# Optimization experiments

Measured on AMD Instinct MI355X. Metric: run time of the kernel, lower is better.

The kernel has to match this reference:

```python
import jax, jax.numpy as jnp
import numpy as np

B, S, H, T, NF = 64, 512, 1024, 4, 12
P = NF * (NF - 1) // 2  # 66 step pairs


def _head(x, w1, b1, w2, b2):
    # LinearsHead (eval mode: dropout = identity): linear -> relu -> linear
    return jax.nn.relu(x @ w1 + b1) @ w2 + b2


def setup_inputs() -> dict:
    key = jax.random.key(0)
    ks = jax.random.split(key, 12)
    sc = 0.02
    # non-overlapping contiguous spans: targets then facts, each L tokens
    L = S // (T + NF)  # 32
    t_start = jnp.arange(T, dtype=jnp.int32) * L
    f_start = (T + jnp.arange(NF, dtype=jnp.int32)) * L
    target_offsets = jnp.broadcast_to(jnp.stack([t_start, t_start + L], -1), (B, T, 2))
    fact_offsets = jnp.broadcast_to(jnp.stack([f_start, f_start + L], -1), (B, NF, 2))
    return {
        'seq_features': jax.random.normal(ks[0], (B, S, H), jnp.float32),
        'cls_features': jax.random.normal(ks[1], (B, H), jnp.float32),
        'target_offsets': target_offsets,
        'fact_offsets': fact_offsets,
        'fact_score_mask': jnp.ones((B, NF, T), jnp.float32),
        'sentsim_w1': sc * jax.random.normal(ks[2], (2 * H, H), jnp.float32),
        'sentsim_b1': jnp.zeros((H,), jnp.float32),
        'sentsim_w2': sc * jax.random.normal(ks[3], (H, 1), jnp.float32),
        'sentsim_b2': jnp.zeros((1,), jnp.float32),
        'step_w1': sc * jax.random.normal(ks[4], (2 * H, H), jnp.float32),
        'step_b1': jnp.zeros((H,), jnp.float32),
        'step_w2': sc * jax.random.normal(ks[5], (H, 1), jnp.float32),
        'step_b2': jnp.zeros((1,), jnp.float32),
        'state_w1': sc * jax.random.normal(ks[6], (H, H), jnp.float32),
        'state_b1': jnp.zeros((H,), jnp.float32),
        'state_w2': sc * jax.random.normal(ks[7], (H, 1), jnp.float32),
        'state_b2': jnp.zeros((1,), jnp.float32),
        'abd_w1': sc * jax.random.normal(ks[8], (2 * H, H), jnp.float32),
        'abd_b1': jnp.zeros((H,), jnp.float32),
        'abd_w2': sc * jax.random.normal(ks[9], (H, 1), jnp.float32),
        'abd_b2': jnp.zeros((1,), jnp.float32),
        'lambda_weight': jnp.array([0.5, 0.5], jnp.float32),
    }


def reference(seq_features, cls_features, target_offsets, fact_offsets, fact_score_mask,
              sentsim_w1, sentsim_b1, sentsim_w2, sentsim_b2,
              step_w1, step_b1, step_w2, step_b2,
              state_w1, state_b1, state_w2, state_b2,
              abd_w1, abd_b1, abd_w2, abd_b2, lambda_weight):
    b, s, h = seq_features.shape
    t = target_offsets.shape[1]
    nf = fact_offsets.shape[1]
    pos = jnp.arange(s)

    def seg_mean(offs):  # offs [b,k,2] -> mean-pooled [b,k,h]
        m = ((pos >= offs[..., 0:1]) & (pos < offs[..., 1:2])).astype(seq_features.dtype)
        cnt = (offs[..., 1] - offs[..., 0]).astype(seq_features.dtype)[..., None]
        return jnp.einsum('bks,bsh->bkh', m, seq_features) / cnt

    tgt = seg_mean(target_offsets)  # [b,t,h]
    fct = seg_mean(fact_offsets)    # [b,nf,h]

    # fact-cls pairs ordered target-major: features[ti*nf+fi] = cat(fact, target)
    ff = jnp.broadcast_to(fct[:, None], (b, t, nf, h))
    tt = jnp.broadcast_to(tgt[:, :, None], (b, t, nf, h))
    pair = jnp.concatenate([ff, tt], -1).reshape(b, t * nf, 2 * h)
    fact_score = jax.nn.sigmoid(_head(pair, sentsim_w1, sentsim_b1, sentsim_w2, sentsim_b2)[..., 0])  # [b, t*nf]
    # original does .view(len(facts), len(targets)) on the flat t-major scores
    mat = fact_score.reshape(b, nf, t)
    max_per_fact = jnp.max(mat * fact_score_mask, axis=2)  # [b, nf]
    state_fact = jnp.mean(max_per_fact, axis=1)            # [b]
    state_cls = jax.nn.sigmoid(_head(cls_features, state_w1, state_b1, state_w2, state_b2)[..., 0])
    w = jax.nn.softmax(lambda_weight)
    state = w[0] * state_fact + w[1] * state_cls           # [b]

    # step pairs: combinations(range(nf), 2) == row-major triu indices
    i1, i2 = jnp.triu_indices(nf, k=1)
    step_feat = jnp.concatenate([fct[:, i1], fct[:, i2]], -1)  # [b,P,2h]
    step = _head(step_feat, step_w1, step_b1, step_w2, step_b2)[..., 0]  # [b,P]

    tside = jnp.mean(tgt, axis=1)  # sum/len over targets [b,h]
    abd_feat = jnp.concatenate([jnp.broadcast_to(tside[:, None], (b, nf, h)), fct], -1)
    abd = _head(abd_feat, abd_w1, abd_b1, abd_w2, abd_b2)[..., 0]  # [b,nf]

    # step_func == 'softmax_all': joint softmax over step + abd scores
    allsc = jax.nn.softmax(jnp.concatenate([step, abd], axis=1), axis=1)
    np_pairs = i1.shape[0]
    step, abd = allsc[:, :np_pairs], allsc[:, np_pairs:]

    # pack: [state | fact_score | step | step_abd]
    return jnp.concatenate([state[:, None], fact_score, step, abd], axis=1)
```

## Files before the change

kernel.cpp:

```cpp
#include <hip/hip_runtime.h>
#include <hip/hip_bf16.h>

#define B_    64
#define S_    512
#define H_    1024
#define HH_   (H_*H_)
#define T_    4
#define NF_   12
#define TNF_  48
#define NP_   66
#define OUTC_ 127

#define NSENT_ (B_*TNF_)
#define NSTEP_ (B_*NP_)
#define NABD_  (B_*NF_)
#define NCLS_  (B_)
#define NWAVES_ (NSENT_+NSTEP_+NABD_+NCLS_)

#define AROW_FCT   0
#define AROW_TGT   768
#define AROW_TSD   1024
#define AROW_CLS   1088
#define AROWS_     1152

#define GROW_FSENT 0
#define GROW_S1    768
#define GROW_S2    1536
#define GROW_AF    2304
#define GROW_TSENT 3072
#define GROW_AT    3328
#define GROW_CLS   3392
#define GROWS_     3456

typedef __bf16 bf16x8 __attribute__((ext_vector_type(8)));
typedef float  f32x4  __attribute__((ext_vector_type(4)));
typedef __attribute__((address_space(1))) const unsigned int gcu32;
typedef __attribute__((address_space(3))) unsigned int lu32;

__device__ __forceinline__ ushort f2bf(float x) {
    union { float f; unsigned u; } c; c.f = x;
    unsigned r = c.u + 0x7fffu + ((c.u >> 16) & 1u);
    return (ushort)(r >> 16);
}
__device__ __forceinline__ float bflo(unsigned u) {
    union { unsigned u; float f; } c; c.u = u << 16; return c.f;
}
__device__ __forceinline__ float bfhi(unsigned u) {
    union { unsigned u; float f; } c; c.u = u & 0xffff0000u; return c.f;
}

__global__ __launch_bounds__(256) void prep_kernel(
    const float* __restrict__ seq, const int* __restrict__ toffs,
    const int* __restrict__ foffs, const float* __restrict__ cls,
    const float* __restrict__ sw1, const float* __restrict__ pw1,
    const float* __restrict__ aw1, const float* __restrict__ cw1,
    float* __restrict__ tgt32, ushort* __restrict__ Abf,
    ushort* __restrict__ Wt)
{
    int blk = blockIdx.x;
    int tid = threadIdx.x;

    if (blk < 1024) {
        int b = blk >> 4;
        int k = blk & 15;
        int start, end, arow;
        float* dst32 = nullptr;
        if (k < T_) {
            start = toffs[(b*T_ + k)*2];
            end   = toffs[(b*T_ + k)*2 + 1];
            dst32 = tgt32 + (size_t)(b*T_ + k) * H_;
            arow  = AROW_TGT + b*T_ + k;
        } else {
            int f = k - T_;
            start = foffs[(b*NF_ + f)*2];
            end   = foffs[(b*NF_ + f)*2 + 1];
            arow  = AROW_FCT + b*NF_ + f;
        }
        int h0 = tid * 4;
        const float* base = seq + ((size_t)b * S_ + start) * H_ + h0;
        float4 s = make_float4(0.f, 0.f, 0.f, 0.f);
        int n = end - start;
        #pragma unroll 4
        for (int r = 0; r < n; ++r) {
            float4 v = *(const float4*)(base + (size_t)r * H_);
            s.x += v.x; s.y += v.y; s.z += v.z; s.w += v.w;
        }
        float inv = 1.f / (float)n;
        s.x *= inv; s.y *= inv; s.z *= inv; s.w *= inv;
        if (dst32) *(float4*)(dst32 + h0) = s;
        ushort4 q; q.x = f2bf(s.x); q.y = f2bf(s.y); q.z = f2bf(s.z); q.w = f2bf(s.w);
        *(ushort4*)(Abf + (size_t)arow * H_ + h0) = q;
    } else if (blk < 1088) {
        int b = blk - 1024;
        int h0 = tid * 4;
        float4 c = *(const float4*)(cls + (size_t)b * H_ + h0);
        ushort4 qc; qc.x = f2bf(c.x); qc.y = f2bf(c.y); qc.z = f2bf(c.z); qc.w = f2bf(c.w);
        *(ushort4*)(Abf + (size_t)(AROW_CLS + b) * H_ + h0) = qc;
    } else {
        __shared__ float Tt[32][33];
        int idx2 = blk - 1088;
        int z = idx2 >> 10;
        int rem = idx2 & 1023;
        int k0 = (rem >> 5) * 32;
        int n0 = (rem & 31) * 32;
        const float* src;
        switch (z) {
            case 0: src = sw1; break;
            case 1: src = pw1; break;
            case 2: src = pw1 + HH_; break;
            case 3: src = aw1 + HH_; break;
            case 4: src = sw1 + HH_; break;
            case 5: src = aw1; break;
            default: src = cw1; break;
        }
        int ty = tid >> 3, tx = tid & 7;
        float4 v = *(const float4*)(src + (size_t)(k0 + ty) * H_ + n0 + tx*4);
        Tt[ty][tx*4 + 0] = v.x; Tt[ty][tx*4 + 1] = v.y;
        Tt[ty][tx*4 + 2] = v.z; Tt[ty][tx*4 + 3] = v.w;
        __syncthreads();
        int nx = ty, kx = tx;
        ushort4 q;
        q.x = f2bf(Tt[kx*4 + 0][nx]); q.y = f2bf(Tt[kx*4 + 1][nx]);
        q.z = f2bf(Tt[kx*4 + 2][nx]); q.w = f2bf(Tt[kx*4 + 3][nx]);
        *(ushort4*)(Wt + (size_t)z * HH_ + (size_t)(n0 + nx) * H_ + k0 + kx*4) = q;
    }
}

__global__ __launch_bounds__(256) void tside_kernel(
    const float* __restrict__ tgt32, ushort* __restrict__ Abf)
{
    int b = blockIdx.x;
    int h0 = threadIdx.x * 4;
    float4 s = make_float4(0.f, 0.f, 0.f, 0.f);
    for (int t = 0; t < T_; ++t) {
        float4 v = *(const float4*)(tgt32 + (size_t)(b*T_ + t)*H_ + h0);
        s.x += v.x; s.y += v.y; s.z += v.z; s.w += v.w;
    }
    ushort4 q;
    q.x = f2bf(s.x*0.25f); q.y = f2bf(s.y*0.25f);
    q.z = f2bf(s.z*0.25f); q.w = f2bf(s.w*0.25f);
    *(ushort4*)(Abf + (size_t)(AROW_TSD + b) * H_ + h0) = q;
}

__global__ __launch_bounds__(128) void gemm_bf16_kernel(
    const ushort* __restrict__ Abf, const ushort* __restrict__ Wt,
    ushort* __restrict__ G)
{
    __shared__ __align__(16) ushort As[64*32];
    __shared__ __align__(16) ushort Bs[64*32];

    const int mt = blockIdx.x;
    const int n0 = blockIdx.y * 64;

    int arow, wsel, grow;
    if (mt < 48)      { wsel = mt / 12; int m = mt % 12;
                        arow = AROW_FCT + m*64; grow = wsel*768 + m*64; }
    else if (mt < 52) { wsel = 4; arow = AROW_TGT + (mt-48)*64;
                        grow = GROW_TSENT + (mt-48)*64; }
    else if (mt == 52){ wsel = 5; arow = AROW_TSD; grow = GROW_AT; }
    else              { wsel = 6; arow = AROW_CLS; grow = GROW_CLS; }

    const int tid  = threadIdx.x;
    const int lane = tid & 63;
    const int w    = tid >> 6;

    const int srow = lane >> 2;
    const int scol = ((lane & 3) ^ ((lane >> 3) & 3)) * 8;
    const ushort* gA0 = Abf + (size_t)(arow + w*32 + srow) * H_ + scol;
    const ushort* gA1 = gA0 + (size_t)16 * H_;
    const ushort* gB0 = Wt + (size_t)wsel * HH_
                        + (size_t)(n0 + w*32 + srow) * H_ + scol;
    const ushort* gB1 = gB0 + (size_t)16 * H_;
    ushort* ldsA = As + w * 1024;
    ushort* ldsB = Bs + w * 1024;

    const int frr  = lane & 15;
    const int c0   = lane >> 4;
    const int swz8 = (c0 ^ ((frr >> 1) & 3)) * 8;
    const int offA = (w*32 + frr) * 32 + swz8;
    const int offB = frr * 32 + swz8;

    f32x4 acc[2][4];
    #pragma unroll
    for (int i = 0; i < 2; ++i)
        #pragma unroll
        for (int j = 0; j < 4; ++j)
            acc[i][j] = (f32x4){0.f, 0.f, 0.f, 0.f};

    #pragma unroll 1
    for (int t = 0; t < 32; ++t) {
        const int kk = t * 32;
        __syncthreads();
        __builtin_amdgcn_global_load_lds((gcu32*)(gA0 + kk), (lu32*)ldsA,         16, 0, 0);
        __builtin_amdgcn_global_load_lds((gcu32*)(gA1 + kk), (lu32*)(ldsA + 512), 16, 0, 0);
        __builtin_amdgcn_global_load_lds((gcu32*)(gB0 + kk), (lu32*)ldsB,         16, 0, 0);
        __builtin_amdgcn_global_load_lds((gcu32*)(gB1 + kk), (lu32*)(ldsB + 512), 16, 0, 0);
        __syncthreads();

        bf16x8 a0 = *(const bf16x8*)(As + offA);
        bf16x8 a1 = *(const bf16x8*)(As + offA + 512);
        bf16x8 b0 = *(const bf16x8*)(Bs + offB);
        bf16x8 b1 = *(const bf16x8*)(Bs + offB + 512);
        bf16x8 b2 = *(const bf16x8*)(Bs + offB + 1024);
        bf16x8 b3 = *(const bf16x8*)(Bs + offB + 1536);

        acc[0][0] = __builtin_amdgcn_mfma_f32_16x16x32_bf16(a0, b0, acc[0][0], 0, 0, 0);
        acc[0][1] = __builtin_amdgcn_mfma_f32_16x16x32_bf16(a0, b1, acc[0][1], 0, 0, 0);
        acc[0][2] = __builtin_amdgcn_mfma_f32_16x16x32_bf16(a0, b2, acc[0][2], 0, 0, 0);
        acc[0][3] = __builtin_amdgcn_mfma_f32_16x16x32_bf16(a0, b3, acc[0][3], 0, 0, 0);
        acc[1][0] = __builtin_amdgcn_mfma_f32_16x16x32_bf16(a1, b0, acc[1][0], 0, 0, 0);
        acc[1][1] = __builtin_amdgcn_mfma_f32_16x16x32_bf16(a1, b1, acc[1][1], 0, 0, 0);
        acc[1][2] = __builtin_amdgcn_mfma_f32_16x16x32_bf16(a1, b2, acc[1][2], 0, 0, 0);
        acc[1][3] = __builtin_amdgcn_mfma_f32_16x16x32_bf16(a1, b3, acc[1][3], 0, 0, 0);
    }

    const int r0 = (lane >> 4) * 4;
    const int cc = lane & 15;
    #pragma unroll
    for (int i = 0; i < 2; ++i) {
        #pragma unroll
        for (int r = 0; r < 4; ++r) {
            size_t gr = (size_t)(grow + w*32 + i*16 + r0 + r) * H_ + n0 + cc;
            #pragma unroll
            for (int j = 0; j < 4; ++j)
                G[gr + j*16] = f2bf(acc[i][j][r]);
        }
    }
}

__global__ __launch_bounds__(256) void combine_kernel(
    const ushort* __restrict__ G,
    const float* __restrict__ sb1, const float* __restrict__ sw2,
    const float* __restrict__ pb1, const float* __restrict__ pw2,
    const float* __restrict__ ab1, const float* __restrict__ aw2,
    const float* __restrict__ cb1, const float* __restrict__ cw2,
    float* __restrict__ ssent, float* __restrict__ sstep,
    float* __restrict__ sabd, float* __restrict__ scls)
{
    int wv = blockIdx.x * 4 + (threadIdx.x >> 6);
    int lane = threadIdx.x & 63;
    if (wv >= NWAVES_) return;

    const ushort *U, *V;
    const float *b1, *w2;
    float* outp;
    if (wv < NSENT_) {
        int b = wv / TNF_, q = wv % TNF_;
        int t = q / NF_, f = q % NF_;
        U = G + (size_t)(GROW_FSENT + b*NF_ + f) * H_;
        V = G + (size_t)(GROW_TSENT + b*T_ + t) * H_;
        b1 = sb1; w2 = sw2; outp = ssent + wv;
    } else if (wv < NSENT_ + NSTEP_) {
        int s = wv - NSENT_;
        int b = s / NP_, p = s % NP_;
        int i = 0, rem = p, cnt = NF_ - 1;
        while (rem >= cnt) { rem -= cnt; --cnt; ++i; }
        int j = i + 1 + rem;
        U = G + (size_t)(GROW_S1 + b*NF_ + i) * H_;
        V = G + (size_t)(GROW_S2 + b*NF_ + j) * H_;
        b1 = pb1; w2 = pw2; outp = sstep + s;
    } else if (wv < NSENT_ + NSTEP_ + NABD_) {
        int s = wv - NSENT_ - NSTEP_;
        int b = s / NF_, f = s % NF_;
        U = G + (size_t)(GROW_AT + b) * H_;
        V = G + (size_t)(GROW_AF + b*NF_ + f) * H_;
        b1 = ab1; w2 = aw2; outp = sabd + s;
    } else {
        int b = wv - NSENT_ - NSTEP_ - NABD_;
        U = G + (size_t)(GROW_CLS + b) * H_;
        V = nullptr;
        b1 = cb1; w2 = cw2; outp = scls + b;
    }

    float acc = 0.f;
    #pragma unroll
    for (int h = 0; h < 2; ++h) {
        int nb = h * 512 + lane * 8;
        uint4 uu = *(const uint4*)(U + nb);
        float us[8] = { bflo(uu.x), bfhi(uu.x), bflo(uu.y), bfhi(uu.y),
                        bflo(uu.z), bfhi(uu.z), bflo(uu.w), bfhi(uu.w) };
        if (V) {
            uint4 vv = *(const uint4*)(V + nb);
            us[0] += bflo(vv.x); us[1] += bfhi(vv.x);
            us[2] += bflo(vv.y); us[3] += bfhi(vv.y);
            us[4] += bflo(vv.z); us[5] += bfhi(vv.z);
            us[6] += bflo(vv.w); us[7] += bfhi(vv.w);
        }
        float4 bA = *(const float4*)(b1 + nb);
        float4 bB = *(const float4*)(b1 + nb + 4);
        float4 wA = *(const float4*)(w2 + nb);
        float4 wB = *(const float4*)(w2 + nb + 4);
        acc = fmaf(fmaxf(us[0] + bA.x, 0.f), wA.x, acc);
        acc = fmaf(fmaxf(us[1] + bA.y, 0.f), wA.y, acc);
        acc = fmaf(fmaxf(us[2] + bA.z, 0.f), wA.z, acc);
        acc = fmaf(fmaxf(us[3] + bA.w, 0.f), wA.w, acc);
        acc = fmaf(fmaxf(us[4] + bB.x, 0.f), wB.x, acc);
        acc = fmaf(fmaxf(us[5] + bB.y, 0.f), wB.y, acc);
        acc = fmaf(fmaxf(us[6] + bB.z, 0.f), wB.z, acc);
        acc = fmaf(fmaxf(us[7] + bB.w, 0.f), wB.w, acc);
    }
    #pragma unroll
    for (int msk = 1; msk < 64; msk <<= 1)
        acc += __shfl_xor(acc, msk);
    if (lane == 0) *outp = acc;
}

__global__ __launch_bounds__(128) void finalize_kernel(
    const float* __restrict__ s_sent, const float* __restrict__ s_step,
    const float* __restrict__ s_abd, const float* __restrict__ s_cls,
    const float* __restrict__ mask, const float* __restrict__ lam,
    const float* __restrict__ sent_b2, const float* __restrict__ step_b2,
    const float* __restrict__ state_b2, const float* __restrict__ abd_b2,
    float* __restrict__ out)
{
    int b = blockIdx.x;
    int tid = threadIdx.x;
    __shared__ float fs[TNF_];
    __shared__ float sc[NP_ + NF_];
    __shared__ float mpf[NF_];
    __shared__ float smax, ssum;

    if (tid < TNF_) {
        float v = 1.f / (1.f + expf(-(s_sent[b*TNF_ + tid] + sent_b2[0])));
        fs[tid] = v;
        out[(size_t)b*OUTC_ + 1 + tid] = v;
    }
    if (tid < NP_)
        sc[tid] = s_step[b*NP_ + tid] + step_b2[0];
    else if (tid < NP_ + NF_)
        sc[tid] = s_abd[b*NF_ + (tid - NP_)] + abd_b2[0];
    __syncthreads();

    if (tid < NF_) {
        float m = -1e30f;
        for (int j = 0; j < T_; ++j)
            m = fmaxf(m, fs[tid*T_ + j] * mask[((size_t)b*NF_ + tid)*T_ + j]);
        mpf[tid] = m;
    }
    __syncthreads();

    if (tid == 0) {
        float sf = 0.f;
        for (int i = 0; i < NF_; ++i) sf += mpf[i];
        sf *= (1.f / NF_);
        float scls2 = 1.f / (1.f + expf(-(s_cls[b] + state_b2[0])));
        float l0 = lam[0], l1 = lam[1];
        float mx = fmaxf(l0, l1);
        float e0 = expf(l0 - mx), e1 = expf(l1 - mx);
        float w0 = e0 / (e0 + e1);
        out[(size_t)b*OUTC_] = w0 * sf + (1.f - w0) * scls2;
        float m2 = -1e30f;
        for (int i = 0; i < NP_ + NF_; ++i) m2 = fmaxf(m2, sc[i]);
        smax = m2;
    }
    __syncthreads();
    if (tid < NP_ + NF_) sc[tid] = expf(sc[tid] - smax);
    __syncthreads();
    if (tid == 0) {
        float s2 = 0.f;
        for (int i = 0; i < NP_ + NF_; ++i) s2 += sc[i];
        ssum = s2;
    }
    __syncthreads();
    if (tid < NP_ + NF_)
        out[(size_t)b*OUTC_ + 1 + TNF_ + tid] = sc[tid] / ssum;
}

extern "C" void kernel_launch(void* const* d_in, const int* in_sizes, int n_in,
                              void* d_out, int out_size, void* d_ws, size_t ws_size,
                              hipStream_t stream)
{
    (void)in_sizes; (void)n_in; (void)out_size; (void)ws_size;
    const float* seq  = (const float*)d_in[0];
    const float* cls  = (const float*)d_in[1];
    const int*   toff = (const int*)d_in[2];
    const int*   foff = (const int*)d_in[3];
    const float* mask = (const float*)d_in[4];
    const float* sw1  = (const float*)d_in[5];
    const float* sb1  = (const float*)d_in[6];
    const float* sw2  = (const float*)d_in[7];
    const float* sb2  = (const float*)d_in[8];
    const float* pw1  = (const float*)d_in[9];
    const float* pb1  = (const float*)d_in[10];
    const float* pw2  = (const float*)d_in[11];
    const float* pb2  = (const float*)d_in[12];
    const float* cw1  = (const float*)d_in[13];
    const float* cb1  = (const float*)d_in[14];
    const float* cw2  = (const float*)d_in[15];
    const float* cb2  = (const float*)d_in[16];
    const float* aw1  = (const float*)d_in[17];
    const float* ab1  = (const float*)d_in[18];
    const float* aw2  = (const float*)d_in[19];
    const float* ab2  = (const float*)d_in[20];
    const float* lam  = (const float*)d_in[21];

    char* wsb = (char*)d_ws;
    float*  tgt32 = (float*)wsb;
    float*  ssent = (float*)(wsb + (1u<<20));
    float*  sstep = ssent + NSENT_;
    float*  sabd  = sstep + NSTEP_;
    float*  scls  = sabd + NABD_;
    ushort* Abf   = (ushort*)(wsb + (1u<<20) + 32768);
    ushort* Wt    = Abf + (size_t)AROWS_ * H_;
    ushort* G     = Wt + (size_t)7 * HH_;

    prep_kernel<<<1088 + 7*1024, 256, 0, stream>>>(
        seq, toff, foff, cls, sw1, pw1, aw1, cw1, tgt32, Abf, Wt);

    tside_kernel<<<B_, 256, 0, stream>>>(tgt32, Abf);

    gemm_bf16_kernel<<<dim3(54, 16), 128, 0, stream>>>(Abf, Wt, G);

    combine_kernel<<<(NWAVES_ + 3) / 4, 256, 0, stream>>>(
        G, sb1, sw2, pb1, pw2, ab1, aw2, cb1, cw2,
        ssent, sstep, sabd, scls);

    finalize_kernel<<<B_, 128, 0, stream>>>(
        ssent, sstep, sabd, scls, mask, lam, sb2, pb2, cb2, ab2, (float*)d_out);
}
```

Baseline: 65.07 us.

## Fold target-side mean into prep kernel and stage combine rows in LDS

The separate tside kernel and its fp32 target scratch buffer are removed. 64 extra prep blocks now recompute the target-span means directly from seq and write the averaged target row. The combine kernel is restructured to one block per (batch, score kind). Each block copies its 14–24 G rows into shared memory once, and its waves then evaluate all pair scores from LDS instead of re-reading the same rows from global memory per wave. This drops one launch and duplicate global reads. In exchange, the target spans are read again from seq, and combine runs with only 192 blocks and 48KB of LDS each.

```diff
diff --git a/kernel.cpp b/kernel.cpp
--- a/kernel.cpp
+++ b/kernel.cpp
@@ -15,7 +15,6 @@
 #define NSTEP_ (B_*NP_)
 #define NABD_  (B_*NF_)
 #define NCLS_  (B_)
-#define NWAVES_ (NSENT_+NSTEP_+NABD_+NCLS_)
 
 #define AROW_FCT   0
 #define AROW_TGT   768
@@ -54,8 +53,7 @@
     const int* __restrict__ foffs, const float* __restrict__ cls,
     const float* __restrict__ sw1, const float* __restrict__ pw1,
     const float* __restrict__ aw1, const float* __restrict__ cw1,
-    float* __restrict__ tgt32, ushort* __restrict__ Abf,
-    ushort* __restrict__ Wt)
+    ushort* __restrict__ Abf, ushort* __restrict__ Wt)
 {
     int blk = blockIdx.x;
     int tid = threadIdx.x;
@@ -64,11 +62,9 @@
         int b = blk >> 4;
         int k = blk & 15;
         int start, end, arow;
-        float* dst32 = nullptr;
         if (k < T_) {
             start = toffs[(b*T_ + k)*2];
             end   = toffs[(b*T_ + k)*2 + 1];
-            dst32 = tgt32 + (size_t)(b*T_ + k) * H_;
             arow  = AROW_TGT + b*T_ + k;
         } else {
             int f = k - T_;
@@ -86,9 +82,9 @@
             s.x += v.x; s.y += v.y; s.z += v.z; s.w += v.w;
         }
         float inv = 1.f / (float)n;
-        s.x *= inv; s.y *= inv; s.z *= inv; s.w *= inv;
-        if (dst32) *(float4*)(dst32 + h0) = s;
-        ushort4 q; q.x = f2bf(s.x); q.y = f2bf(s.y); q.z = f2bf(s.z); q.w = f2bf(s.w);
+        ushort4 q;
+        q.x = f2bf(s.x*inv); q.y = f2bf(s.y*inv);
+        q.z = f2bf(s.z*inv); q.w = f2bf(s.w*inv);
         *(ushort4*)(Abf + (size_t)arow * H_ + h0) = q;
     } else if (blk < 1088) {
         int b = blk - 1024;
@@ -96,7 +92,7 @@
         float4 c = *(const float4*)(cls + (size_t)b * H_ + h0);
         ushort4 qc; qc.x = f2bf(c.x); qc.y = f2bf(c.y); qc.z = f2bf(c.z); qc.w = f2bf(c.w);
         *(ushort4*)(Abf + (size_t)(AROW_CLS + b) * H_ + h0) = qc;
-    } else {
+    } else if (blk < 8256) {
         __shared__ float Tt[32][33];
         int idx2 = blk - 1088;
         int z = idx2 >> 10;
@@ -123,23 +119,31 @@
         q.x = f2bf(Tt[kx*4 + 0][nx]); q.y = f2bf(Tt[kx*4 + 1][nx]);
         q.z = f2bf(Tt[kx*4 + 2][nx]); q.w = f2bf(Tt[kx*4 + 3][nx]);
         *(ushort4*)(Wt + (size_t)z * HH_ + (size_t)(n0 + nx) * H_ + k0 + kx*4) = q;
-    }
-}
-
-__global__ __launch_bounds__(256) void tside_kernel(
-    const float* __restrict__ tgt32, ushort* __restrict__ Abf)
-{
-    int b = blockIdx.x;
-    int h0 = threadIdx.x * 4;
-    float4 s = make_float4(0.f, 0.f, 0.f, 0.f);
-    for (int t = 0; t < T_; ++t) {
-        float4 v = *(const float4*)(tgt32 + (size_t)(b*T_ + t)*H_ + h0);
-        s.x += v.x; s.y += v.y; s.z += v.z; s.w += v.w;
-    }
-    ushort4 q;
-    q.x = f2bf(s.x*0.25f); q.y = f2bf(s.y*0.25f);
-    q.z = f2bf(s.z*0.25f); q.w = f2bf(s.w*0.25f);
-    *(ushort4*)(Abf + (size_t)(AROW_TSD + b) * H_ + h0) = q;
+    } else {
+        int b = blk - 8256;
+        int h0 = tid * 4;
+        float4 acc = make_float4(0.f, 0.f, 0.f, 0.f);
+        #pragma unroll
+        for (int t = 0; t < T_; ++t) {
+            int start = toffs[(b*T_ + t)*2];
+            int end   = toffs[(b*T_ + t)*2 + 1];
+            const float* base = seq + ((size_t)b * S_ + start) * H_ + h0;
+            float4 s = make_float4(0.f, 0.f, 0.f, 0.f);
+            int n = end - start;
+            #pragma unroll 4
+            for (int r = 0; r < n; ++r) {
+                float4 v = *(const float4*)(base + (size_t)r * H_);
+                s.x += v.x; s.y += v.y; s.z += v.z; s.w += v.w;
+            }
+            float inv = 1.f / (float)n;
+            acc.x += s.x*inv; acc.y += s.y*inv;
+            acc.z += s.z*inv; acc.w += s.w*inv;
+        }
+        ushort4 q;
+        q.x = f2bf(acc.x*0.25f); q.y = f2bf(acc.y*0.25f);
+        q.z = f2bf(acc.z*0.25f); q.w = f2bf(acc.w*0.25f);
+        *(ushort4*)(Abf + (size_t)(AROW_TSD + b) * H_ + h0) = q;
+    }
 }
 
 __global__ __launch_bounds__(128) void gemm_bf16_kernel(
@@ -237,72 +241,85 @@
     float* __restrict__ ssent, float* __restrict__ sstep,
     float* __restrict__ sabd, float* __restrict__ scls)
 {
-    int wv = blockIdx.x * 4 + (threadIdx.x >> 6);
-    int lane = threadIdx.x & 63;
-    if (wv >= NWAVES_) return;
-
-    const ushort *U, *V;
-    const float *b1, *w2;
-    float* outp;
-    if (wv < NSENT_) {
-        int b = wv / TNF_, q = wv % TNF_;
-        int t = q / NF_, f = q % NF_;
-        U = G + (size_t)(GROW_FSENT + b*NF_ + f) * H_;
-        V = G + (size_t)(GROW_TSENT + b*T_ + t) * H_;
-        b1 = sb1; w2 = sw2; outp = ssent + wv;
-    } else if (wv < NSENT_ + NSTEP_) {
-        int s = wv - NSENT_;
-        int b = s / NP_, p = s % NP_;
-        int i = 0, rem = p, cnt = NF_ - 1;
-        while (rem >= cnt) { rem -= cnt; --cnt; ++i; }
-        int j = i + 1 + rem;
-        U = G + (size_t)(GROW_S1 + b*NF_ + i) * H_;
-        V = G + (size_t)(GROW_S2 + b*NF_ + j) * H_;
-        b1 = pb1; w2 = pw2; outp = sstep + s;
-    } else if (wv < NSENT_ + NSTEP_ + NABD_) {
-        int s = wv - NSENT_ - NSTEP_;
-        int b = s / NF_, f = s % NF_;
-        U = G + (size_t)(GROW_AT + b) * H_;
-        V = G + (size_t)(GROW_AF + b*NF_ + f) * H_;
-        b1 = ab1; w2 = aw2; outp = sabd + s;
-    } else {
-        int b = wv - NSENT_ - NSTEP_ - NABD_;
-        U = G + (size_t)(GROW_CLS + b) * H_;
-        V = nullptr;
-        b1 = cb1; w2 = cw2; outp = scls + b;
-    }
-
-    float acc = 0.f;
-    #pragma unroll
-    for (int h = 0; h < 2; ++h) {
-        int nb = h * 512 + lane * 8;
-        uint4 uu = *(const uint4*)(U + nb);
-        float us[8] = { bflo(uu.x), bfhi(uu.x), bflo(uu.y), bfhi(uu.y),
-                        bflo(uu.z), bfhi(uu.z), bflo(uu.w), bfhi(uu.w) };
-        if (V) {
-            uint4 vv = *(const uint4*)(V + nb);
-            us[0] += bflo(vv.x); us[1] += bfhi(vv.x);
-            us[2] += bflo(vv.y); us[3] += bfhi(vv.y);
-            us[4] += bflo(vv.z); us[5] += bfhi(vv.z);
-            us[6] += bflo(vv.w); us[7] += bfhi(vv.w);
-        }
-        float4 bA = *(const float4*)(b1 + nb);
-        float4 bB = *(const float4*)(b1 + nb + 4);
-        float4 wA = *(const float4*)(w2 + nb);
-        float4 wB = *(const float4*)(w2 + nb + 4);
-        acc = fmaf(fmaxf(us[0] + bA.x, 0.f), wA.x, acc);
-        acc = fmaf(fmaxf(us[1] + bA.y, 0.f), wA.y, acc);
-        acc = fmaf(fmaxf(us[2] + bA.z, 0.f), wA.z, acc);
-        acc = fmaf(fmaxf(us[3] + bA.w, 0.f), wA.w, acc);
-        acc = fmaf(fmaxf(us[4] + bB.x, 0.f), wB.x, acc);
-        acc = fmaf(fmaxf(us[5] + bB.y, 0.f), wB.y, acc);
-        acc = fmaf(fmaxf(us[6] + bB.z, 0.f), wB.z, acc);
-        acc = fmaf(fmaxf(us[7] + bB.w, 0.f), wB.w, acc);
-    }
-    #pragma unroll
-    for (int msk = 1; msk < 64; msk <<= 1)
-        acc += __shfl_xor(acc, msk);
-    if (lane == 0) *outp = acc;
+    __shared__ __align__(16) ushort rows[24 * 1024];
+
+    const int b    = blockIdx.x;
+    const int kind = blockIdx.y;
+    const int tid  = threadIdx.x;
+    const int wv   = tid >> 6;
+    const int lane = tid & 63;
+
+    const int nrows = (kind == 0) ? 16 : (kind == 1) ? 24 : 14;
+
+    for (int r = 0; r < nrows; ++r) {
+        int gi;
+        if (kind == 0)      gi = (r < 12) ? (GROW_FSENT + b*NF_ + r)
+                                          : (GROW_TSENT + b*T_ + (r - 12));
+        else if (kind == 1) gi = (r < 12) ? (GROW_S1 + b*NF_ + r)
+                                          : (GROW_S2 + b*NF_ + (r - 12));
+        else                gi = (r < 12) ? (GROW_AF + b*NF_ + r)
+                                          : ((r == 12) ? (GROW_AT + b)
+                                                       : (GROW_CLS + b));
+        *(uint2*)(rows + r*1024 + tid*4) =
+            *(const uint2*)(G + (size_t)gi * H_ + tid*4);
+    }
+    __syncthreads();
+
+    const int nsc = (kind == 0) ? TNF_ : (kind == 1) ? NP_ : 13;
+    for (int s = wv; s < nsc; s += 4) {
+        const ushort *U, *V;
+        const float *b1, *w2;
+        float* outp;
+        if (kind == 0) {
+            int t = s / NF_, f = s % NF_;
+            U = rows + f*1024; V = rows + (12 + t)*1024;
+            b1 = sb1; w2 = sw2; outp = ssent + b*TNF_ + s;
+        } else if (kind == 1) {
+            int i = 0, rem = s, cnt = NF_ - 1;
+            while (rem >= cnt) { rem -= cnt; --cnt; ++i; }
+            int j = i + 1 + rem;
+            U = rows + i*1024; V = rows + (12 + j)*1024;
+            b1 = pb1; w2 = pw2; outp = sstep + b*NP_ + s;
+        } else if (s < 12) {
+            U = rows + 12*1024; V = rows + s*1024;
+            b1 = ab1; w2 = aw2; outp = sabd + b*NF_ + s;
+        } else {
+            U = rows + 13*1024; V = nullptr;
+            b1 = cb1; w2 = cw2; outp = scls + b;
+        }
+
+        float acc = 0.f;
+        #pragma unroll
+        for (int h = 0; h < 2; ++h) {
+            int nb = h * 512 + lane * 8;
+            uint4 uu = *(const uint4*)(U + nb);
+            float us[8] = { bflo(uu.x), bfhi(uu.x), bflo(uu.y), bfhi(uu.y),
+                            bflo(uu.z), bfhi(uu.z), bflo(uu.w), bfhi(uu.w) };
+            if (V) {
+                uint4 vv = *(const uint4*)(V + nb);
+                us[0] += bflo(vv.x); us[1] += bfhi(vv.x);
+                us[2] += bflo(vv.y); us[3] += bfhi(vv.y);
+                us[4] += bflo(vv.z); us[5] += bfhi(vv.z);
+                us[6] += bflo(vv.w); us[7] += bfhi(vv.w);
+            }
+            float4 bA = *(const float4*)(b1 + nb);
+            float4 bB = *(const float4*)(b1 + nb + 4);
+            float4 wA = *(const float4*)(w2 + nb);
+            float4 wB = *(const float4*)(w2 + nb + 4);
+            acc = fmaf(fmaxf(us[0] + bA.x, 0.f), wA.x, acc);
+            acc = fmaf(fmaxf(us[1] + bA.y, 0.f), wA.y, acc);
+            acc = fmaf(fmaxf(us[2] + bA.z, 0.f), wA.z, acc);
+            acc = fmaf(fmaxf(us[3] + bA.w, 0.f), wA.w, acc);
+            acc = fmaf(fmaxf(us[4] + bB.x, 0.f), wB.x, acc);
+            acc = fmaf(fmaxf(us[5] + bB.y, 0.f), wB.y, acc);
+            acc = fmaf(fmaxf(us[6] + bB.z, 0.f), wB.z, acc);
+            acc = fmaf(fmaxf(us[7] + bB.w, 0.f), wB.w, acc);
+        }
+        #pragma unroll
+        for (int msk = 1; msk < 64; msk <<= 1)
+            acc += __shfl_xor(acc, msk);
+        if (lane == 0) *outp = acc;
+    }
 }
 
 __global__ __launch_bounds__(128) void finalize_kernel(
@@ -395,23 +412,20 @@
     const float* lam  = (const float*)d_in[21];
 
     char* wsb = (char*)d_ws;
-    float*  tgt32 = (float*)wsb;
-    float*  ssent = (float*)(wsb + (1u<<20));
+    float*  ssent = (float*)wsb;
     float*  sstep = ssent + NSENT_;
     float*  sabd  = sstep + NSTEP_;
     float*  scls  = sabd + NABD_;
-    ushort* Abf   = (ushort*)(wsb + (1u<<20) + 32768);
+    ushort* Abf   = (ushort*)(wsb + 65536);
     ushort* Wt    = Abf + (size_t)AROWS_ * H_;
     ushort* G     = Wt + (size_t)7 * HH_;
 
-    prep_kernel<<<1088 + 7*1024, 256, 0, stream>>>(
-        seq, toff, foff, cls, sw1, pw1, aw1, cw1, tgt32, Abf, Wt);
-
-    tside_kernel<<<B_, 256, 0, stream>>>(tgt32, Abf);
+    prep_kernel<<<8320, 256, 0, stream>>>(
+        seq, toff, foff, cls, sw1, pw1, aw1, cw1, Abf, Wt);
 
     gemm_bf16_kernel<<<dim3(54, 16), 128, 0, stream>>>(Abf, Wt, G);
 
-    combine_kernel<<<(NWAVES_ + 3) / 4, 256, 0, stream>>>(
+    combine_kernel<<<dim3(B_, 3), 256, 0, stream>>>(
         G, sb1, sw2, pb1, pw2, ab1, aw2, cb1, cw2,
         ssent, sstep, sabd, scls);
 
```

Result: slower. 89.80 us (+38.0%).
